# Kernel tuning notes

Measured on AMD Instinct MI355X. Metric: run time of the kernel, lower is better.

## Reference

```python
import jax, jax.numpy as jnp
import numpy as np

B, Q, K, D, H, DH = 4, 512, 4096, 1024, 8, 128  # qk_channels=v_channels=out=1024

def setup_inputs() -> dict:
    key = jax.random.key(0)
    ks = jax.random.split(key, 5)
    s = 1.0 / np.sqrt(D)
    return {
        "inputs_q": jax.random.normal(ks[0], (B, Q, D), jnp.float32),
        "inputs_kv": jax.random.normal(ks[1], (B, K, D), jnp.float32),
        "Wq": jax.random.normal(ks[2], (D, H, DH), jnp.float32) * s,
        "Wkv": jax.random.normal(ks[3], (D, H, 2 * DH), jnp.float32) * s,
        "Wproj": jax.random.normal(ks[4], (H, DH, D), jnp.float32) * (1.0 / np.sqrt(H * DH)),
        "b_proj": jnp.zeros((D,), jnp.float32),
    }

def reference(inputs_q, inputs_kv, Wq, Wkv, Wproj, b_proj):
    # QKV projections (no bias)
    q = jnp.einsum('bqd,dhe->bqhe', inputs_q, Wq)          # [B,Q,H,DH]
    kv = jnp.einsum('bkd,dhe->bkhe', inputs_kv, Wkv)        # [B,K,H,2*DH]
    k, v = kv[..., :DH], kv[..., DH:]
    # scaled dot-product attention (softmax in fp32, per source)
    attn = jnp.einsum('bqhd,bkhd->bhqk', q, k) / np.sqrt(DH)
    attn = jax.nn.softmax(attn.astype(jnp.float32), axis=-1).astype(v.dtype)
    o = jnp.einsum('bhqk,bkhd->bqhd', attn, v)              # [B,Q,H,DH]
    # output projection contracting (head, head_dim), with bias
    return jnp.einsum('bqhd,hdo->bqo', o, Wproj) + b_proj   # [B,Q,D]
```

## Files before the change

kernel.cpp:

```cpp
#include <hip/hip_runtime.h>
#include <hip/hip_bf16.h>
#include <cstdint>

typedef unsigned short u16;
typedef unsigned int u32;
typedef __bf16 bf16x8 __attribute__((ext_vector_type(8)));
typedef u16 u16x8 __attribute__((ext_vector_type(8)));
typedef u16 u16x4 __attribute__((ext_vector_type(4)));
typedef float f32x4 __attribute__((ext_vector_type(4)));

#define MFMA16(a, b, c) __builtin_amdgcn_mfma_f32_16x16x32_bf16(a, b, c, 0, 0, 0)

__device__ __forceinline__ void async16(const void* g, void* s) {
    __builtin_amdgcn_global_load_lds((const __attribute__((address_space(1))) void*)g,
                                     (__attribute__((address_space(3))) void*)s, 16, 0, 0);
}

__device__ __forceinline__ u16 f2bf(float f) {
    u32 u; __builtin_memcpy(&u, &f, 4);
    u = u + 0x7fffu + ((u >> 16) & 1u);
    return (u16)(u >> 16);
}

__global__ __launch_bounds__(256) void convert_inputs(const float* __restrict__ inq,
                                                      u16* __restrict__ Aq,
                                                      const float* __restrict__ inkv,
                                                      u16* __restrict__ Akv) {
    const int blk = blockIdx.x;
    const float* in; u16* out; size_t i;
    if (blk < 1024) { in = inq;  out = Aq;  i = (size_t)blk * 256 + threadIdx.x; }
    else            { in = inkv; out = Akv; i = (size_t)(blk - 1024) * 256 + threadIdx.x; }
    const float4* p = (const float4*)in + i * 2;
    const float4 a = p[0], b = p[1];
    u16x8 v;
    v[0] = f2bf(a.x); v[1] = f2bf(a.y); v[2] = f2bf(a.z); v[3] = f2bf(a.w);
    v[4] = f2bf(b.x); v[5] = f2bf(b.y); v[6] = f2bf(b.z); v[7] = f2bf(b.w);
    ((u16x8*)out)[i] = v;
}

__global__ __launch_bounds__(256) void prep_weights(const float* __restrict__ Wq,  u16* __restrict__ WqT,
                                                    const float* __restrict__ Wkv, u16* __restrict__ WkvT,
                                                    const float* __restrict__ Wp,  u16* __restrict__ WpT) {
    __shared__ u16 t[64][65];
    const int blk = blockIdx.x;
    const float* in; u16* out; int R, C, bx, by;
    if (blk < 256)      { in = Wq;  out = WqT;  R = 1024; C = 1024; bx = blk & 15;  by = blk >> 4; }
    else if (blk < 768) { in = Wkv; out = WkvT; R = 1024; C = 2048; bx = (blk - 256) & 31; by = (blk - 256) >> 5; }
    else                { in = Wp;  out = WpT;  R = 1024; C = 1024; bx = (blk - 768) & 15; by = (blk - 768) >> 4; }
    const int r0 = by << 6, c0 = bx << 6;
    const int tid = threadIdx.x;
#pragma unroll
    for (int i = 0; i < 16; i++) {
        int idx = i * 256 + tid;
        int r = idx >> 6, c = idx & 63;
        t[r][c] = f2bf(in[(size_t)(r0 + r) * C + c0 + c]);
    }
    __syncthreads();
#pragma unroll
    for (int i = 0; i < 16; i++) {
        int idx = i * 256 + tid;
        int c = idx >> 6, r = idx & 63;
        out[(size_t)(c0 + c) * R + r0 + r] = t[r][c];
    }
}

template <bool OUTF32, int NT>
__global__ __launch_bounds__(256) void gemm_bt(const u16* __restrict__ A,
                                               const u16* __restrict__ B,
                                               void* __restrict__ Cv,
                                               const float* __restrict__ bias,
                                               int M, int N, int K) {
    constexpr int NJ = NT / 32;
    __shared__ __align__(16) u16 As[128 * 64];
    __shared__ __align__(16) u16 Bs[NT * 64];
    const int tid = threadIdx.x;
    const int wave = tid >> 6, lane = tid & 63;
    const int lrow = lane & 15, quad = lane >> 4;
    const int nb = N / NT;
    const int bx = blockIdx.x % nb, by = blockIdx.x / nb;
    const long m0 = (long)by << 7, n0 = (long)bx * NT;
    const int wm = (wave >> 1) << 6, wn = (wave & 1) * (NT / 2);

    const f32x4 fz = {0.f, 0.f, 0.f, 0.f};
    f32x4 acc[4][NJ];
#pragma unroll
    for (int i = 0; i < 4; i++)
#pragma unroll
        for (int j = 0; j < NJ; j++) acc[i][j] = fz;

    const int srow = wave * 8 + (lane >> 3);
    const int scol = ((lane & 7) ^ (lane >> 3)) << 3;
    const u16* Ag = A + (m0 + srow) * K + scol;
    const u16* Bg = B + (n0 + srow) * K + scol;
    u16* AsW = &As[wave * 512];
    u16* BsW = &Bs[wave * 512];

    for (int k0 = 0; k0 < K; k0 += 64) {
        __syncthreads();
#pragma unroll
        for (int c = 0; c < 4; c++)
            async16(Ag + (long)c * 32 * K + k0, AsW + c * 2048);
#pragma unroll
        for (int c = 0; c < NT / 32; c++)
            async16(Bg + (long)c * 32 * K + k0, BsW + c * 2048);
        __syncthreads();
#pragma unroll
        for (int c = 0; c < 2; c++) {
            bf16x8 af[4], bfr[NJ];
#pragma unroll
            for (int i = 0; i < 4; i++) {
                const int row = wm + i * 16 + lrow;
                af[i] = *(const bf16x8*)&As[row * 64 + (((c * 4 + quad) ^ (row & 7)) << 3)];
            }
#pragma unroll
            for (int j = 0; j < NJ; j++) {
                const int row = wn + j * 16 + lrow;
                bfr[j] = *(const bf16x8*)&Bs[row * 64 + (((c * 4 + quad) ^ (row & 7)) << 3)];
            }
#pragma unroll
            for (int i = 0; i < 4; i++)
#pragma unroll
                for (int j = 0; j < NJ; j++)
                    acc[i][j] = MFMA16(af[i], bfr[j], acc[i][j]);
        }
    }
#pragma unroll
    for (int j = 0; j < NJ; j++) {
        const long col = n0 + wn + j * 16 + lrow;
        const float bv = bias ? bias[col] : 0.0f;
#pragma unroll
        for (int i = 0; i < 4; i++) {
            const long row = m0 + wm + i * 16 + quad * 4;
#pragma unroll
            for (int r = 0; r < 4; r++) {
                const float v = acc[i][j][r] + bv;
                if (OUTF32) ((float*)Cv)[(row + r) * N + col] = v;
                else        ((u16*)Cv)[(row + r) * N + col] = f2bf(v);
            }
        }
    }
}

__global__ __launch_bounds__(512, 2) void gemm_kv256(const u16* __restrict__ A,
                                                     const u16* __restrict__ B,
                                                     u16* __restrict__ C,
                                                     u16* __restrict__ Vt) {
    constexpr int K = 1024, N = 2048, NT = 16;
    __shared__ __align__(16) u16 As[2][256 * 64];
    __shared__ __align__(16) u16 Bs[2][256 * 64];
    const int tid = threadIdx.x;
    const int wave = tid >> 6, lane = tid & 63;
    const int lrow = lane & 15, quad = lane >> 4;
    const int wMi = wave >> 2, wNi = wave & 3;
    const int wm = wMi * 128, wn = wNi * 64;
    const int wg = blockIdx.x;
    const int swz = (wg & 7) * 64 + (wg >> 3);
    const int bx = swz & 7, by = swz >> 3;
    const long m0 = (long)by << 8, n0 = (long)bx << 8;

    const int srow = tid >> 3;
    const int scol = ((tid & 7) ^ (srow & 7)) << 3;
    const u16* Ag = A + (m0 + srow) * K + scol;
    const u16* Bg = B + (n0 + srow) * K + scol;
    const int sdst = tid * 8;

    auto stgA = [&](int bi, int h, int kt) {
        async16(Ag + (size_t)(h * 128) * K + kt * 64,      &As[bi][h * 8192 + sdst]);
        async16(Ag + (size_t)(h * 128 + 64) * K + kt * 64, &As[bi][h * 8192 + 4096 + sdst]);
    };
    auto stgB = [&](int bi, int h, int kt) {
        async16(Bg + (size_t)(h * 128) * K + kt * 64,      &Bs[bi][h * 8192 + sdst]);
        async16(Bg + (size_t)(h * 128 + 64) * K + kt * 64, &Bs[bi][h * 8192 + 4096 + sdst]);
    };

    stgB(0, 0, 0); stgB(0, 1, 0); stgA(0, 0, 0); stgA(0, 1, 0);
    stgB(1, 0, 1); stgB(1, 1, 1); stgA(1, 0, 1);

    const f32x4 fz = {0.f, 0.f, 0.f, 0.f};
    f32x4 acc[8][4];
#pragma unroll
    for (int i = 0; i < 8; i++)
#pragma unroll
        for (int j = 0; j < 4; j++) acc[i][j] = fz;

    asm volatile("s_waitcnt vmcnt(6)" ::: "memory");
    __builtin_amdgcn_s_barrier();

    bf16x8 av[4][2], bv[4][2];
    for (int t = 0; t < NT; ++t) {
        const int cur = t & 1, nxt = cur ^ 1;
#pragma unroll
        for (int i = 0; i < 4; i++) {
            const int row = wm + i * 16 + lrow;
#pragma unroll
            for (int c = 0; c < 2; c++)
                av[i][c] = *(const bf16x8*)&As[cur][row * 64 + (((c * 4 + quad) ^ (row & 7)) << 3)];
        }
#pragma unroll
        for (int j = 0; j < 4; j++) {
            const int row = wn + j * 16 + lrow;
#pragma unroll
            for (int c = 0; c < 2; c++)
                bv[j][c] = *(const bf16x8*)&Bs[cur][row * 64 + (((c * 4 + quad) ^ (row & 7)) << 3)];
        }
        if (t + 1 < NT) stgA(nxt, 1, t + 1);
        __builtin_amdgcn_s_barrier();
        asm volatile("s_waitcnt lgkmcnt(0)" ::: "memory");
        __builtin_amdgcn_s_setprio(1);
#pragma unroll
        for (int i = 0; i < 4; i++)
#pragma unroll
            for (int j = 0; j < 2; j++)
#pragma unroll
                for (int c = 0; c < 2; c++)
                    acc[i][j] = MFMA16(av[i][c], bv[j][c], acc[i][j]);
        __builtin_amdgcn_s_setprio(0);
        __builtin_amdgcn_s_barrier();
        if (t + 2 < NT) stgB(cur, 0, t + 2);
        __builtin_amdgcn_s_barrier();
        __builtin_amdgcn_s_setprio(1);
#pragma unroll
        for (int i = 0; i < 4; i++)
#pragma unroll
            for (int j = 2; j < 4; j++)
#pragma unroll
                for (int c = 0; c < 2; c++)
                    acc[i][j] = MFMA16(av[i][c], bv[j][c], acc[i][j]);
        __builtin_amdgcn_s_setprio(0);
        __builtin_amdgcn_s_barrier();
#pragma unroll
        for (int i = 0; i < 4; i++) {
            const int row = wm + (i + 4) * 16 + lrow;
#pragma unroll
            for (int c = 0; c < 2; c++)
                av[i][c] = *(const bf16x8*)&As[cur][row * 64 + (((c * 4 + quad) ^ (row & 7)) << 3)];
        }
        if (t + 2 < NT) stgB(cur, 1, t + 2);
        __builtin_amdgcn_s_barrier();
        asm volatile("s_waitcnt lgkmcnt(0)" ::: "memory");
        __builtin_amdgcn_s_setprio(1);
#pragma unroll
        for (int i = 0; i < 4; i++)
#pragma unroll
            for (int j = 0; j < 2; j++)
#pragma unroll
                for (int c = 0; c < 2; c++)
                    acc[i + 4][j] = MFMA16(av[i][c], bv[j][c], acc[i + 4][j]);
        __builtin_amdgcn_s_setprio(0);
        __builtin_amdgcn_s_barrier();
        if (t + 2 < NT) stgA(cur, 0, t + 2);
        __builtin_amdgcn_s_barrier();
        __builtin_amdgcn_s_setprio(1);
#pragma unroll
        for (int i = 0; i < 4; i++)
#pragma unroll
            for (int j = 2; j < 4; j++)
#pragma unroll
                for (int c = 0; c < 2; c++)
                    acc[i + 4][j] = MFMA16(av[i][c], bv[j][c], acc[i + 4][j]);
        __builtin_amdgcn_s_setprio(0);
        if (t + 2 < NT)      { asm volatile("s_waitcnt vmcnt(6)" ::: "memory"); }
        else if (t + 1 < NT) { asm volatile("s_waitcnt vmcnt(0)" ::: "memory"); }
        __builtin_amdgcn_s_barrier();
    }

    const int h = bx;
    if (wNi < 2) {
#pragma unroll
        for (int j = 0; j < 4; j++) {
            const long col = n0 + wn + j * 16 + lrow;
#pragma unroll
            for (int i = 0; i < 8; i++) {
                const long row = m0 + wm + i * 16 + quad * 4;
#pragma unroll
                for (int r = 0; r < 4; r++)
                    C[(row + r) * N + col] = f2bf(acc[i][j][r]);
            }
        }
    } else {
#pragma unroll
        for (int j = 0; j < 4; j++) {
            const int dh = (wNi - 2) * 64 + j * 16 + lrow;
#pragma unroll
            for (int i = 0; i < 8; i++) {
                const int row = (int)m0 + wm + i * 16 + quad * 4;
                const int b = row >> 12, kv = row & 4095;
                u16x4 pk;
#pragma unroll
                for (int r = 0; r < 4; r++) pk[r] = f2bf(acc[i][j][r]);
                *(u16x4*)&Vt[(((size_t)b * 8 + h) * 128 + dh) * 4096 + kv] = pk;
            }
        }
    }
}

__global__ __launch_bounds__(512) void flash_attn_split(const u16* __restrict__ qb,
                                                        const u16* __restrict__ kvb,
                                                        const u16* __restrict__ vTb,
                                                        float* __restrict__ Opart,
                                                        float* __restrict__ Mpart,
                                                        float* __restrict__ Lpart) {
    __shared__ __align__(16) u16 Ks[64 * 128];
    __shared__ __align__(16) u16 Vs[128 * 64];
    __shared__ __align__(16) u16 Ps[8][16 * 64];
    const int tid = threadIdx.x, wave = tid >> 6, lane = tid & 63;
    const int lrow = lane & 15, quad = lane >> 4;
    const int blk = blockIdx.x;
    const int split = blk & 3, qt = (blk >> 2) & 3, h = (blk >> 4) & 7, b = blk >> 7;
    const int q0 = qt * 128;
    const int kbase = split * 1024;

    bf16x8 qf[4];
    {
        const u16* qp = qb + (((size_t)(b * 512 + q0 + wave * 16 + lrow) * 8 + h) << 7) + quad * 8;
#pragma unroll
        for (int c = 0; c < 4; c++) qf[c] = *(const bf16x8*)(qp + c * 32);
    }

    const f32x4 fz = {0.f, 0.f, 0.f, 0.f};
    f32x4 oacc[8];
#pragma unroll
    for (int g = 0; g < 8; g++) oacc[g] = fz;
    float mrow = -1e30f, lsum = 0.f;
    const float scale = 0.08838834764831845f;

    const int kRow = tid >> 4, kBlk = tid & 15;
    const int vRow = tid >> 3, vBlk = tid & 7;
    const u16* kg = kvb + (size_t)b * 4096 * 2048 + h * 256 + kBlk * 8;
    const u16* vg = vTb + (size_t)(b * 8 + h) * 128 * 4096 + vBlk * 8;

    for (int k0 = kbase; k0 < kbase + 1024; k0 += 64) {
        __syncthreads();
#pragma unroll
        for (int i = 0; i < 2; i++) {
            const int r = i * 32 + kRow;
            *(bf16x8*)&Ks[r * 128 + ((kBlk ^ (r & 15)) << 3)] =
                *(const bf16x8*)&kg[(size_t)(k0 + r) * 2048];
            const int rv = i * 64 + vRow;
            *(bf16x8*)&Vs[rv * 64 + ((vBlk ^ (rv & 7)) << 3)] =
                *(const bf16x8*)&vg[(size_t)rv * 4096 + k0];
        }
        __syncthreads();

        f32x4 s[4];
#pragma unroll
        for (int t = 0; t < 4; t++) {
            f32x4 a = fz;
#pragma unroll
            for (int c = 0; c < 4; c++) {
                const bf16x8 kf = *(const bf16x8*)
                    &Ks[(t * 16 + lrow) * 128 + (((c * 4 + quad) ^ lrow) << 3)];
                a = MFMA16(kf, qf[c], a);
            }
            s[t] = a * scale;
        }

        float mx = s[0][0];
#pragma unroll
        for (int t = 0; t < 4; t++)
#pragma unroll
            for (int r = 0; r < 4; r++) mx = fmaxf(mx, s[t][r]);
        mx = fmaxf(mx, __shfl_xor(mx, 16));
        mx = fmaxf(mx, __shfl_xor(mx, 32));
        const float mn = fmaxf(mrow, mx);
        const float alpha = __expf(mrow - mn);
        mrow = mn;
        float sum = 0.f;
#pragma unroll
        for (int t = 0; t < 4; t++)
#pragma unroll
            for (int r = 0; r < 4; r++) {
                float p = __expf(s[t][r] - mn);
                s[t][r] = p;
                sum += p;
            }
        sum += __shfl_xor(sum, 16);
        sum += __shfl_xor(sum, 32);
        lsum = lsum * alpha + sum;

        u16* Pw = &Ps[wave][0];
#pragma unroll
        for (int t = 0; t < 4; t++) {
            u16x4 pk;
#pragma unroll
            for (int r = 0; r < 4; r++) pk[r] = f2bf(s[t][r]);
            const int kvo = t * 16 + quad * 4;
            *(u16x4*)&Pw[lrow * 64 + (((kvo >> 3) ^ (lrow & 7)) << 3) + (kvo & 7)] = pk;
        }
        asm volatile("s_waitcnt lgkmcnt(0)" ::: "memory");
        const bf16x8 pf0 = *(const bf16x8*)&Pw[lrow * 64 + ((quad ^ (lrow & 7)) << 3)];
        const bf16x8 pf1 = *(const bf16x8*)&Pw[lrow * 64 + (((4 + quad) ^ (lrow & 7)) << 3)];

#pragma unroll
        for (int g = 0; g < 8; g++) {
            f32x4 o = oacc[g] * alpha;
            o = MFMA16(*(const bf16x8*)&Vs[(g * 16 + lrow) * 64 + ((quad ^ (lrow & 7)) << 3)], pf0, o);
            o = MFMA16(*(const bf16x8*)&Vs[(g * 16 + lrow) * 64 + (((4 + quad) ^ (lrow & 7)) << 3)], pf1, o);
            oacc[g] = o;
        }
    }

    float* Ob = Opart + (size_t)blk * 16384;
#pragma unroll
    for (int g = 0; g < 8; g++)
        *(f32x4*)&Ob[(wave * 16 + lrow) * 128 + g * 16 + quad * 4] = oacc[g];
    if (quad == 0) {
        const int row = blk * 128 + wave * 16 + lrow;
        Mpart[row] = mrow;
        Lpart[row] = lsum;
    }
}

__global__ __launch_bounds__(512) void combine_attn(const float* __restrict__ Opart,
                                                    const float* __restrict__ Mpart,
                                                    const float* __restrict__ Lpart,
                                                    u16* __restrict__ ob) {
    const int c = blockIdx.x;
    const int qt = c & 3, h = (c >> 2) & 7, b = c >> 5;
    const int lr = threadIdx.x >> 2, cg = (threadIdx.x & 3) * 32;
    float ms[4], w[4];
    float m = -1e30f;
#pragma unroll
    for (int s = 0; s < 4; s++) { ms[s] = Mpart[(c * 4 + s) * 128 + lr]; m = fmaxf(m, ms[s]); }
    float l = 0.f;
#pragma unroll
    for (int s = 0; s < 4; s++) { w[s] = __expf(ms[s] - m); l += w[s] * Lpart[(c * 4 + s) * 128 + lr]; }
    const float inv = 1.f / l;
#pragma unroll
    for (int s = 0; s < 4; s++) w[s] *= inv;
    const size_t orow = ((size_t)(b * 512 + qt * 128 + lr) * 8 + h) << 7;
#pragma unroll
    for (int j = 0; j < 4; j++) {
        f32x4 a0 = {0.f, 0.f, 0.f, 0.f}, a1 = a0;
#pragma unroll
        for (int s = 0; s < 4; s++) {
            const f32x4* p = (const f32x4*)(Opart + ((size_t)(c * 4 + s)) * 16384 + (size_t)lr * 128 + cg + j * 8);
            a0 += p[0] * w[s];
            a1 += p[1] * w[s];
        }
        u16x8 v;
#pragma unroll
        for (int i = 0; i < 4; i++) { v[i] = f2bf(a0[i]); v[4 + i] = f2bf(a1[i]); }
        *(u16x8*)&ob[orow + cg + j * 8] = v;
    }
}

extern "C" void kernel_launch(void* const* d_in, const int* in_sizes, int n_in,
                              void* d_out, int out_size, void* d_ws, size_t ws_size,
                              hipStream_t stream) {
    const float* inq   = (const float*)d_in[0];
    const float* inkv  = (const float*)d_in[1];
    const float* Wq    = (const float*)d_in[2];
    const float* Wkv   = (const float*)d_in[3];
    const float* Wproj = (const float*)d_in[4];
    const float* bproj = (const float*)d_in[5];
    float* out = (float*)d_out;

    u16* WqT    = (u16*)d_ws;
    u16* WkvT   = WqT + (size_t)1024 * 1024;
    u16* WprojT = WkvT + (size_t)2048 * 1024;
    u16* Aq     = WprojT + (size_t)1024 * 1024;
    u16* Akv    = Aq + (size_t)2048 * 1024;
    u16* qbuf   = Akv + (size_t)16384 * 1024;
    u16* kvbuf  = qbuf + (size_t)2048 * 1024;
    u16* vTbuf  = kvbuf + (size_t)16384 * 2048;
    u16* obuf   = vTbuf + (size_t)32 * 128 * 4096;

    float* Opart = (float*)Akv;
    float* Mpart = (float*)Aq;
    float* Lpart = Mpart + 65536;

    convert_inputs<<<9216, 256, 0, stream>>>(inq, Aq, inkv, Akv);
    prep_weights<<<1024, 256, 0, stream>>>(Wq, WqT, Wkv, WkvT, Wproj, WprojT);

    gemm_bt<false, 64><<<16 * 16, 256, 0, stream>>>(Aq, WqT, qbuf, nullptr, 2048, 1024, 1024);
    gemm_kv256<<<512, 512, 0, stream>>>(Akv, WkvT, kvbuf, vTbuf);

    flash_attn_split<<<512, 512, 0, stream>>>(qbuf, kvbuf, vTbuf, Opart, Mpart, Lpart);
    combine_attn<<<128, 512, 0, stream>>>(Opart, Mpart, Lpart, obuf);

    gemm_bt<true, 64><<<16 * 16, 256, 0, stream>>>(obuf, WprojT, (void*)out, bproj, 2048, 1024, 1024);
}
```

Measured before the change: 305.1 us.

## Swap MFMA operands for vectorized stores and restructure KV GEMM pipeline

```diff
diff --git a/kernel.cpp b/kernel.cpp
--- a/kernel.cpp
+++ b/kernel.cpp
@@ -121,21 +121,24 @@
             for (int i = 0; i < 4; i++)
 #pragma unroll
                 for (int j = 0; j < NJ; j++)
-                    acc[i][j] = MFMA16(af[i], bfr[j], acc[i][j]);
-        }
-    }
-#pragma unroll
-    for (int j = 0; j < NJ; j++) {
-        const long col = n0 + wn + j * 16 + lrow;
-        const float bv = bias ? bias[col] : 0.0f;
-#pragma unroll
-        for (int i = 0; i < 4; i++) {
-            const long row = m0 + wm + i * 16 + quad * 4;
-#pragma unroll
-            for (int r = 0; r < 4; r++) {
-                const float v = acc[i][j][r] + bv;
-                if (OUTF32) ((float*)Cv)[(row + r) * N + col] = v;
-                else        ((u16*)Cv)[(row + r) * N + col] = f2bf(v);
+                    acc[i][j] = MFMA16(bfr[j], af[i], acc[i][j]);
+        }
+    }
+#pragma unroll
+    for (int i = 0; i < 4; i++) {
+        const long row = m0 + wm + i * 16 + lrow;
+#pragma unroll
+        for (int j = 0; j < NJ; j++) {
+            const long colb = n0 + wn + j * 16 + quad * 4;
+            if (OUTF32) {
+                f32x4 v = acc[i][j];
+                if (bias) v += *(const f32x4*)&bias[colb];
+                *(f32x4*)&((float*)Cv)[row * N + colb] = v;
+            } else {
+                u16x4 pk;
+#pragma unroll
+                for (int r = 0; r < 4; r++) pk[r] = f2bf(acc[i][j][r]);
+                *(u16x4*)&((u16*)Cv)[row * N + colb] = pk;
             }
         }
     }
@@ -153,6 +156,7 @@
     const int lrow = lane & 15, quad = lane >> 4;
     const int wMi = wave >> 2, wNi = wave & 3;
     const int wm = wMi * 128, wn = wNi * 64;
+    const bool kswap = (wNi < 2);
     const int wg = blockIdx.x;
     const int swz = (wg & 7) * 64 + (wg >> 3);
     const int bx = swz & 7, by = swz >> 3;
@@ -164,17 +168,20 @@
     const u16* Bg = B + (n0 + srow) * K + scol;
     const int sdst = tid * 8;
 
-    auto stgA = [&](int bi, int h, int kt) {
-        async16(Ag + (size_t)(h * 128) * K + kt * 64,      &As[bi][h * 8192 + sdst]);
-        async16(Ag + (size_t)(h * 128 + 64) * K + kt * 64, &As[bi][h * 8192 + 4096 + sdst]);
+    auto stgA2 = [&](int bi, int kt) {
+        async16(Ag + (size_t)0 * K + kt * 64,         &As[bi][sdst]);
+        async16(Ag + (size_t)64 * K + kt * 64,        &As[bi][4096 + sdst]);
+        async16(Ag + (size_t)128 * K + kt * 64,       &As[bi][8192 + sdst]);
+        async16(Ag + (size_t)192 * K + kt * 64,       &As[bi][12288 + sdst]);
     };
     auto stgB = [&](int bi, int h, int kt) {
         async16(Bg + (size_t)(h * 128) * K + kt * 64,      &Bs[bi][h * 8192 + sdst]);
         async16(Bg + (size_t)(h * 128 + 64) * K + kt * 64, &Bs[bi][h * 8192 + 4096 + sdst]);
     };
 
-    stgB(0, 0, 0); stgB(0, 1, 0); stgA(0, 0, 0); stgA(0, 1, 0);
-    stgB(1, 0, 1); stgB(1, 1, 1); stgA(1, 0, 1);
+    stgB(0, 0, 0); stgB(0, 1, 0);
+    stgA2(0, 0);
+    stgB(1, 0, 1); stgB(1, 1, 1);
 
     const f32x4 fz = {0.f, 0.f, 0.f, 0.f};
     f32x4 acc[8][4];
@@ -183,98 +190,96 @@
 #pragma unroll
         for (int j = 0; j < 4; j++) acc[i][j] = fz;
 
-    asm volatile("s_waitcnt vmcnt(6)" ::: "memory");
+    asm volatile("s_waitcnt vmcnt(4)" ::: "memory");
     __builtin_amdgcn_s_barrier();
 
-    bf16x8 av[4][2], bv[4][2];
+    bf16x8 av[2][2], bv[4][2];
+    auto cluster = [&](int i0) {
+        if (kswap) {
+#pragma unroll
+            for (int ii = 0; ii < 2; ii++)
+#pragma unroll
+                for (int j = 0; j < 4; j++)
+#pragma unroll
+                    for (int c = 0; c < 2; c++)
+                        acc[i0 + ii][j] = MFMA16(bv[j][c], av[ii][c], acc[i0 + ii][j]);
+        } else {
+#pragma unroll
+            for (int ii = 0; ii < 2; ii++)
+#pragma unroll
+                for (int j = 0; j < 4; j++)
+#pragma unroll
+                    for (int c = 0; c < 2; c++)
+                        acc[i0 + ii][j] = MFMA16(av[ii][c], bv[j][c], acc[i0 + ii][j]);
+        }
+    };
+    auto rdA = [&](int cur, int i0) {
+#pragma unroll
+        for (int ii = 0; ii < 2; ii++) {
+            const int row = wm + (i0 + ii) * 16 + lrow;
+#pragma unroll
+            for (int c = 0; c < 2; c++)
+                av[ii][c] = *(const bf16x8*)&As[cur][row * 64 + (((c * 4 + quad) ^ (row & 7)) << 3)];
+        }
+    };
+
     for (int t = 0; t < NT; ++t) {
         const int cur = t & 1, nxt = cur ^ 1;
 #pragma unroll
-        for (int i = 0; i < 4; i++) {
-            const int row = wm + i * 16 + lrow;
-#pragma unroll
-            for (int c = 0; c < 2; c++)
-                av[i][c] = *(const bf16x8*)&As[cur][row * 64 + (((c * 4 + quad) ^ (row & 7)) << 3)];
-        }
-#pragma unroll
         for (int j = 0; j < 4; j++) {
             const int row = wn + j * 16 + lrow;
 #pragma unroll
             for (int c = 0; c < 2; c++)
                 bv[j][c] = *(const bf16x8*)&Bs[cur][row * 64 + (((c * 4 + quad) ^ (row & 7)) << 3)];
         }
-        if (t + 1 < NT) stgA(nxt, 1, t + 1);
+        rdA(cur, 0);
+        if (t + 1 < NT) stgA2(nxt, t + 1);
+        asm volatile("s_waitcnt lgkmcnt(8)" ::: "memory");
         __builtin_amdgcn_s_barrier();
         asm volatile("s_waitcnt lgkmcnt(0)" ::: "memory");
         __builtin_amdgcn_s_setprio(1);
-#pragma unroll
-        for (int i = 0; i < 4; i++)
-#pragma unroll
-            for (int j = 0; j < 2; j++)
-#pragma unroll
-                for (int c = 0; c < 2; c++)
-                    acc[i][j] = MFMA16(av[i][c], bv[j][c], acc[i][j]);
+        cluster(0);
         __builtin_amdgcn_s_setprio(0);
         __builtin_amdgcn_s_barrier();
+        rdA(cur, 2);
         if (t + 2 < NT) stgB(cur, 0, t + 2);
-        __builtin_amdgcn_s_barrier();
-        __builtin_amdgcn_s_setprio(1);
-#pragma unroll
-        for (int i = 0; i < 4; i++)
-#pragma unroll
-            for (int j = 2; j < 4; j++)
-#pragma unroll
-                for (int c = 0; c < 2; c++)
-                    acc[i][j] = MFMA16(av[i][c], bv[j][c], acc[i][j]);
-        __builtin_amdgcn_s_setprio(0);
-        __builtin_amdgcn_s_barrier();
-#pragma unroll
-        for (int i = 0; i < 4; i++) {
-            const int row = wm + (i + 4) * 16 + lrow;
-#pragma unroll
-            for (int c = 0; c < 2; c++)
-                av[i][c] = *(const bf16x8*)&As[cur][row * 64 + (((c * 4 + quad) ^ (row & 7)) << 3)];
-        }
-        if (t + 2 < NT) stgB(cur, 1, t + 2);
         __builtin_amdgcn_s_barrier();
         asm volatile("s_waitcnt lgkmcnt(0)" ::: "memory");
         __builtin_amdgcn_s_setprio(1);
-#pragma unroll
-        for (int i = 0; i < 4; i++)
-#pragma unroll
-            for (int j = 0; j < 2; j++)
-#pragma unroll
-                for (int c = 0; c < 2; c++)
-                    acc[i + 4][j] = MFMA16(av[i][c], bv[j][c], acc[i + 4][j]);
+        cluster(2);
         __builtin_amdgcn_s_setprio(0);
         __builtin_amdgcn_s_barrier();
-        if (t + 2 < NT) stgA(cur, 0, t + 2);
-        __builtin_amdgcn_s_barrier();
+        rdA(cur, 4);
+        if (t + 2 < NT) stgB(cur, 1, t + 2);
+        __builtin_amdgcn_s_barrier();
+        asm volatile("s_waitcnt lgkmcnt(0)" ::: "memory");
         __builtin_amdgcn_s_setprio(1);
-#pragma unroll
-        for (int i = 0; i < 4; i++)
-#pragma unroll
-            for (int j = 2; j < 4; j++)
-#pragma unroll
-                for (int c = 0; c < 2; c++)
-                    acc[i + 4][j] = MFMA16(av[i][c], bv[j][c], acc[i + 4][j]);
+        cluster(4);
         __builtin_amdgcn_s_setprio(0);
-        if (t + 2 < NT)      { asm volatile("s_waitcnt vmcnt(6)" ::: "memory"); }
+        __builtin_amdgcn_s_barrier();
+        rdA(cur, 6);
+        __builtin_amdgcn_s_barrier();
+        asm volatile("s_waitcnt lgkmcnt(0)" ::: "memory");
+        __builtin_amdgcn_s_setprio(1);
+        cluster(6);
+        __builtin_amdgcn_s_setprio(0);
+        if (t + 2 < NT)      { asm volatile("s_waitcnt vmcnt(4)" ::: "memory"); }
         else if (t + 1 < NT) { asm volatile("s_waitcnt vmcnt(0)" ::: "memory"); }
         __builtin_amdgcn_s_barrier();
     }
 
     const int h = bx;
-    if (wNi < 2) {
-#pragma unroll
-        for (int j = 0; j < 4; j++) {
-            const long col = n0 + wn + j * 16 + lrow;
-#pragma unroll
-            for (int i = 0; i < 8; i++) {
-                const long row = m0 + wm + i * 16 + quad * 4;
-#pragma unroll
-                for (int r = 0; r < 4; r++)
-                    C[(row + r) * N + col] = f2bf(acc[i][j][r]);
+    if (kswap) {
+#pragma unroll
+        for (int i = 0; i < 8; i++) {
+            const long row = m0 + wm + i * 16 + lrow;
+#pragma unroll
+            for (int j = 0; j < 4; j++) {
+                const long colb = n0 + wn + j * 16 + quad * 4;
+                u16x4 pk;
+#pragma unroll
+                for (int r = 0; r < 4; r++) pk[r] = f2bf(acc[i][j][r]);
+                *(u16x4*)&C[row * N + colb] = pk;
             }
         }
     } else {
```

Result: slower. 312.1 us (+2.3%).
